# Kernel tuning notes

Measured on AMD Instinct MI355X. Metric: run time of the kernel, lower is better.

Reference implementation:

```python
import jax, jax.numpy as jnp
import numpy as np
from jax.scipy.special import logsumexp

NG, NF, NR, NW = 5, 5, 5, 4
STEP = 1 + NG + NF + NR            # 16 signatures per writer
M_OTH = NG + NF + NR               # comparisons per writer
MARGIN, RANDOM_MARGIN = 1.0, 1.5
ALPHA, BETA, P_W, R_W = 0.1, 1.0, 0.01, 0.01
GAMMA = 5.0                        # SoftDTW(gamma=5, bandwidth=int(0.1)=0 -> full DTW)
KNUM, KMUL = 5, 2.0
MAXLEN, FEAT = 512, 64
BIG = 1e10                         # finite stand-in for +inf (exp(-BIG/GAMMA) == 0 in f32)


def _pairwise_sqdist(X, Y):
    # X,Y: (B, L, F) -> (B, L, L) squared euclidean cost (SoftDTW distance func)
    xy = jnp.einsum('bif,bjf->bij', X, Y)
    d = (X * X).sum(-1)[:, :, None] + (Y * Y).sum(-1)[:, None, :] - 2.0 * xy
    return jnp.maximum(d, 0.0)


def _soft_dtw(D, la, lb):
    # Batched soft-DTW via anti-diagonal scan. Padded DP is causal, so
    # R[la, lb] only depends on D[:la, :lb]; padding never contaminates it.
    B, L, _ = D.shape
    ii = jnp.arange(1, L + 1)
    r2 = jnp.full((B, L + 1), BIG, D.dtype).at[:, 0].set(0.0)  # diag d=0: R[0,0]=0
    r1 = jnp.full((B, L + 1), BIG, D.dtype)                    # diag d=1: borders

    def step(carry, d):
        rp2, rp1 = carry
        j = d - ii
        valid = (j >= 1) & (j <= L)
        jc = jnp.clip(j, 1, L)
        Dd = D[:, ii - 1, jc - 1]                               # (B, L)
        # softmin(R[i-1,j], R[i,j-1], R[i-1,j-1]) = -g*logsumexp(-r/g)
        stack = jnp.stack([-rp1[:, :-1], -rp1[:, 1:], -rp2[:, :-1]]) / GAMMA
        smin = -GAMMA * logsumexp(stack, axis=0)
        vals = jnp.where(valid[None, :], Dd + smin, BIG)
        r_new = jnp.concatenate([jnp.full((B, 1), BIG, D.dtype), vals], axis=1)
        return (rp1, r_new), r_new

    _, R = jax.lax.scan(step, (r2, r1), jnp.arange(2, 2 * L + 1))
    # R: (2L-1, B, L+1); diag d stored at d-2, R[la, lb] sits at index la
    return R[la + lb - 2, jnp.arange(B), la]


def _mmd(src, tgt):
    # DAN-style multi-kernel gaussian MMD; signatures flattened to vectors
    b = src.shape[0]
    total = jnp.concatenate([src, tgt], axis=0)
    n = total.shape[0]
    sq = (total * total).sum(-1)
    l2 = jnp.maximum(sq[:, None] + sq[None, :] - 2.0 * (total @ total.T), 0.0)
    bw = jax.lax.stop_gradient(l2.sum()) / (n * n - n)
    bw = bw / KMUL ** (KNUM // 2)
    bws = bw * KMUL ** jnp.arange(KNUM, dtype=total.dtype)
    k = jnp.exp(-l2[None] / bws[:, None, None]).sum(0)
    return jnp.mean(k[:b, :b] + k[b:, b:] - k[:b, b:] - k[b:, :b])


def _forward(data, lens):
    w = jnp.arange(NW)
    anchor_idx = jnp.repeat(w * STEP, M_OTH)
    other_idx = (w[:, None] * STEP + 1 + jnp.arange(M_OTH)[None, :]).reshape(-1)
    D = _pairwise_sqdist(data[anchor_idx], data[other_idx])
    la, lb = lens[anchor_idx], lens[other_idx]
    r = _soft_dtw(D, la, lb)
    dists = (r / (la + lb).astype(data.dtype)).reshape(NW, M_OTH)  # avg pooling
    dist_g = dists[:, :NG]
    dist_n = dists[:, NG:]
    lk_s = jax.nn.relu(dist_g[:, :, None] + MARGIN - dist_n[:, None, :NF])
    lk_r = jax.nn.relu(dist_g[:, :, None] + RANDOM_MARGIN - dist_n[:, None, NF:])
    ca = dist_g.mean(1)
    cb = dist_n[:, :NW].mean(1)            # quirk of original: first nw negatives
    intra = (dist_g - ca[:, None]).sum(1)  # identically 0, kept for fidelity
    inter = jax.nn.relu(BETA - jnp.abs(ca - cb))
    nz_s = (lk_s > 0).sum((1, 2))
    nz_r = (lk_r > 0).sum((1, 2))
    lv = (lk_s.sum((1, 2)) + lk_r.sum((1, 2))) / (nz_s + nz_r + 1)
    # BCE over softmin pairs (dist_g[0], dist_r[j]) vs targets (1, 0):
    # softmin gives sm0 = sigmoid(dr - dg0); BCE = -(log sm0 + log(1-sm1))/2 = -log sm0
    logits = dist_n[:, NF:] - dist_g[:, 0:1]
    bce = -jnp.mean(jax.nn.log_sigmoid(logits), axis=1)
    total_loss = jnp.mean(bce + lv + intra * P_W + inter * R_W)
    # pairwise MMD over writers (i in 0..nw-1, j in 1..nw-1, i != j), nr random excluded
    pairs = np.array([(i, j) for i in range(NW) for j in range(1, NW) if i != j])
    seg = data.reshape(NW, STEP, MAXLEN, FEAT)[:, :STEP - NR]
    seg = seg.reshape(NW, STEP - NR, MAXLEN * FEAT)
    mmd_vals = jax.vmap(_mmd)(seg[pairs[:, 0]], seg[pairs[:, 1]])
    siz = NW * (NW + 1) // 2
    mmds = jnp.zeros((siz,), data.dtype).at[:pairs.shape[0]].set(mmd_vals)
    mmd1 = jnp.max(mmds) * ALPHA
    return total_loss + mmd1, nz_r.sum()


def setup_inputs():
    key = jax.random.key(0)
    k1, k2, k3 = jax.random.split(key, 3)
    data = jax.random.normal(k1, (NW * STEP, MAXLEN, FEAT), dtype=jnp.float32)
    lens = jax.random.randint(k2, (NW * STEP,), MAXLEN // 2, MAXLEN + 1, dtype=jnp.int32)
    target = jax.random.randint(k3, (NW * STEP,), 0, NW, dtype=jnp.int32)
    return {"data": data, "lens": lens, "target": target, "n_classes": 100}


def reference(data, lens, target, n_classes):
    # target / n_classes are unused in the original forward (sms is dead code)
    return _forward(data, lens)
```

## Files before the change

### kernel.cpp

```cpp
#include <hip/hip_runtime.h>
#include <math.h>

#define NG 5
#define NF 5
#define NR 5
#define NW 4
#define STEP 16
#define M_OTH 15
#define NB 60
#define L 512
#define FEAT 64
#define GAMMA 5.0f
#define SEGN 11
#define NSEG 44
#define SEGD 32768

#define C1   0.28853900817779268f
#define GLN2 3.4657359027997265f
#define BIGS 2.8853900e9f
#define BNDW 800
#define GRAM_BLK0 60

__global__ __launch_bounds__(256, 2) void sqdist_kernel(const float* __restrict__ data,
                                                        const int* __restrict__ lens,
                                                        float* __restrict__ DS) {
    int b = blockIdx.z;
    int w = b / M_OTH, m = b % M_OTH;
    int la = lens[w * STEP];
    int lb = lens[w * STEP + 1 + m];
    int ti = blockIdx.y * 128;
    int tj = blockIdx.x * 128;
    if (ti >= la || tj >= lb) return;

    const float* X = data + (size_t)(w * STEP) * L * FEAT;
    const float* Y = data + (size_t)(w * STEP + 1 + m) * L * FEAT;

    __shared__ float Xs[128][68];
    __shared__ float Ys[128][68];
    __shared__ float nx[128], ny[128];

    int t = threadIdx.y * 16 + threadIdx.x;
    #pragma unroll
    for (int k = 0; k < 8; ++k) {
        int idx = t + k * 256;
        int r = idx >> 4, c = (idx & 15) * 4;
        *(float4*)&Xs[r][c] = *(const float4*)(X + (size_t)(ti + r) * FEAT + c);
        *(float4*)&Ys[r][c] = *(const float4*)(Y + (size_t)(tj + r) * FEAT + c);
    }
    __syncthreads();
    {
        int r = t & 127;
        const float* row = (t < 128) ? Xs[r] : Ys[r];
        float s = 0.f;
        #pragma unroll
        for (int f = 0; f < 64; f += 4) {
            float4 v = *(const float4*)&row[f];
            s += v.x * v.x + v.y * v.y + v.z * v.z + v.w * v.w;
        }
        if (t < 128) nx[r] = s; else ny[r] = s;
    }
    __syncthreads();

    int tx = threadIdx.x, ty = threadIdx.y;
    float acc[8][8] = {};
    for (int f = 0; f < 64; f += 4) {
        float4 xv[8], yv[8];
        #pragma unroll
        for (int a = 0; a < 8; ++a) xv[a] = *(const float4*)&Xs[16 * a + tx][f];
        #pragma unroll
        for (int c = 0; c < 8; ++c) yv[c] = *(const float4*)&Ys[16 * c + ty][f];
        #pragma unroll
        for (int a = 0; a < 8; ++a)
            #pragma unroll
            for (int c = 0; c < 8; ++c)
                acc[a][c] += xv[a].x * yv[c].x + xv[a].y * yv[c].y +
                             xv[a].z * yv[c].z + xv[a].w * yv[c].w;
    }
    #pragma unroll
    for (int a = 0; a < 8; ++a) {
        int ii = ti + 16 * a + tx;
        float xn = nx[16 * a + tx];
        #pragma unroll
        for (int c = 0; c < 8; ++c) {
            int jj = tj + 16 * c + ty;
            float d = xn + ny[16 * c + ty] - 2.0f * acc[a][c];
            size_t idx = ((size_t)b * 512 + ((jj + (ii >> 1)) & 511)) * 512 + ii;
            DS[idx] = fmaxf(d, 0.0f) * C1;
        }
    }
}

__device__ __forceinline__ float dpp_shift_up1(float x) {
    int xi = __float_as_int(x);
    int sh  = __builtin_amdgcn_update_dpp(xi, xi, 0x111, 0xF, 0xF, false);
    int b15 = __builtin_amdgcn_update_dpp(xi, xi, 0x142, 0xF, 0xF, false);
    int lane = (int)(threadIdx.x & 63);
    int r = ((lane & 15) == 0) ? b15 : sh;
    return __int_as_float(r);
}

__device__ void gram_body(const float* __restrict__ data, float* __restrict__ Gm, int f) {
    int bx = 0, rem = f;
    for (int q = 0; q < 11; ++q) { int c = 11 - q; if (rem < c) { bx = q; break; } rem -= c; }
    int by = bx + rem;
    int t = threadIdx.x;
    int lane = t & 63, wv = t >> 6;
    const float* pa[4];
    const float* pb[4];
    #pragma unroll
    for (int i = 0; i < 4; ++i) {
        int sa = bx * 4 + i;
        int sb = by * 4 + i;
        pa[i] = data + (size_t)((sa / SEGN) * STEP + (sa % SEGN)) * SEGD;
        pb[i] = data + (size_t)((sb / SEGN) * STEP + (sb % SEGN)) * SEGD;
    }
    float acc[16] = {};
    for (int d = t * 4; d < SEGD; d += 1024) {
        float4 ra[4], rb[4];
        #pragma unroll
        for (int i = 0; i < 4; ++i) ra[i] = *(const float4*)(pa[i] + d);
        #pragma unroll
        for (int i = 0; i < 4; ++i) rb[i] = *(const float4*)(pb[i] + d);
        #pragma unroll
        for (int i = 0; i < 4; ++i)
            #pragma unroll
            for (int jj = 0; jj < 4; ++jj)
                acc[i * 4 + jj] += ra[i].x * rb[jj].x + ra[i].y * rb[jj].y +
                                   ra[i].z * rb[jj].z + ra[i].w * rb[jj].w;
    }
    #pragma unroll
    for (int i = 0; i < 16; ++i)
        #pragma unroll
        for (int s = 32; s > 0; s >>= 1)
            acc[i] += __shfl_xor(acc[i], s);
    __shared__ float part[4][16];
    if (lane == 0)
        #pragma unroll
        for (int i = 0; i < 16; ++i) part[wv][i] = acc[i];
    __syncthreads();
    if (t < 16) {
        float s = part[0][t] + part[1][t] + part[2][t] + part[3][t];
        int a = bx * 4 + (t >> 2), c = by * 4 + (t & 3);
        Gm[a * NSEG + c] = s;
        Gm[c * NSEG + a] = s;
    }
}

__global__ __launch_bounds__(256) void dtw_gram_kernel(const float* __restrict__ DS,
                                                       const int* __restrict__ lens,
                                                       const float* __restrict__ data,
                                                       float* __restrict__ res,
                                                       float* __restrict__ Gm) {
    int blk = blockIdx.x;
    if (blk >= GRAM_BLK0) { gram_body(data, Gm, blk - GRAM_BLK0); return; }

    int b = blk;
    int w_ = b / M_OTH, m = b % M_OTH;
    int la = lens[w_ * STEP];
    int lb = lens[w_ * STEP + 1 + m];
    int tid = threadIdx.x;
    int W = tid >> 6, l = tid & 63, G = tid;
    const float* Db = DS + (size_t)b * 512 * 512;

    __shared__ float bnd[3][BNDW];
    for (int k = tid; k < 3 * BNDW; k += 256)
        ((float*)bnd)[k] = __int_as_float(0x7FC00000);
    __syncthreads();

    int gstar = (la - 1) >> 1;
    int rstar = (la - 1) & 1;
    int tcap = lb + gstar - 1;
    if (64 * W > gstar) return;
    int gmax = min(64 * W + 63, gstar);
    int t0 = 64 * W;
    int tend = lb + gmax - 1;
    int needmax = lb + 64 * W - 1;
    bool pub = (W < 3);

    float nv0 = BIGS, nv1 = BIGS;
    float A0 = BIGS;
    float C0 = (G == 0) ? 0.0f : BIGS;
    float out = 0.0f;

    float2 ring[16];
    #pragma unroll
    for (int k = 0; k < 16; ++k)
        ring[k] = *(const float2*)&Db[(size_t)((t0 + k) & 511) * 512 + 2 * G];
    float ch[16];
    #pragma unroll
    for (int k = 0; k < 16; ++k) ch[k] = __int_as_float(0x7FC00000);

    int j = 1 - l;
    const float* bsrc = (W > 0) ? bnd[W - 1] : bnd[0];

    for (int t = t0; t <= tend; t += 16) {
        if (W > 0 && t <= needmax) {
            int lastIdx = min(t + 15, needmax);
            for (;;) {
                float chk = 0.f;
                #pragma unroll
                for (int k = 0; k < 16; ++k)
                    if (t + k <= needmax) chk += ch[k];
                if (!__builtin_isnan(chk)) break;
                float v = __hip_atomic_load(&bsrc[lastIdx], __ATOMIC_RELAXED,
                                            __HIP_MEMORY_SCOPE_WORKGROUP);
                while (__builtin_isnan(v)) {
                    __builtin_amdgcn_s_sleep(2);
                    v = __hip_atomic_load(&bsrc[lastIdx], __ATOMIC_RELAXED,
                                          __HIP_MEMORY_SCOPE_WORKGROUP);
                }
                __builtin_amdgcn_fence(__ATOMIC_ACQUIRE, "workgroup");
                #pragma unroll
                for (int k = 0; k < 4; ++k) {
                    float4 c = *(const float4*)&bsrc[t + 4 * k];
                    ch[4 * k] = c.x; ch[4 * k + 1] = c.y;
                    ch[4 * k + 2] = c.z; ch[4 * k + 3] = c.w;
                }
            }
        }
        #pragma unroll
        for (int k = 0; k < 16; ++k) {
            int tt = t + k;
            float l0 = BIGS;
            if (W > 0) l0 = (tt <= needmax) ? ch[k] : BIGS;
            A0 = (l == 0) ? l0 : A0;
            float D0 = ring[k].x, D1 = ring[k].y;
            ring[k] = *(const float2*)&Db[(size_t)((tt + 16) & 511) * 512 + 2 * G];
            float m2a = fminf(nv0, C0), mxa = fmaxf(nv0, C0);
            float E2a = 1.0f + __builtin_amdgcn_exp2f(m2a - mxa);
            float m2b = fminf(nv1, nv0), mxb = fmaxf(nv1, nv0);
            float E2b = 1.0f + __builtin_amdgcn_exp2f(m2b - mxb);
            float mn0 = fminf(A0, m2a);
            float s0 = __builtin_amdgcn_exp2f(mn0 - A0) +
                       E2a * __builtin_amdgcn_exp2f(mn0 - m2a);
            float t0v = D0 + (mn0 - __builtin_amdgcn_logf(s0));
            float mn1 = fminf(t0v, m2b);
            float s1 = __builtin_amdgcn_exp2f(mn1 - t0v) +
                       E2b * __builtin_amdgcn_exp2f(mn1 - m2b);
            float t1v = D1 + (mn1 - __builtin_amdgcn_logf(s1));
            bool valid = (unsigned)(j - 1) < (unsigned)L;
            nv0 = valid ? t0v : nv0;
            nv1 = valid ? t1v : nv1;
            if (tt == tcap) { if (G == gstar) out = rstar ? nv1 : nv0; }
            float up = dpp_shift_up1(nv1);
            if (pub && l == 63)
                __hip_atomic_store(&bnd[W][tt + 1], nv1, __ATOMIC_RELAXED,
                                   __HIP_MEMORY_SCOPE_WORKGROUP);
            C0 = A0;
            A0 = up;
            j += 1;
        }
        if (W > 0) {
            #pragma unroll
            for (int k = 0; k < 4; ++k) {
                float4 c = *(const float4*)&bsrc[t + 16 + 4 * k];
                ch[4 * k] = c.x; ch[4 * k + 1] = c.y;
                ch[4 * k + 2] = c.z; ch[4 * k + 3] = c.w;
            }
        }
    }
    if (G == gstar) res[b] = out * GLN2 / (float)(la + lb);
}

__global__ __launch_bounds__(512) void finalize_kernel(const float* __restrict__ res,
                                                       const float* __restrict__ G,
                                                       float* __restrict__ out) {
    __shared__ float wpart[9][8];
    __shared__ float bws[9];
    __shared__ float mmds[9];
    __shared__ float wloss[NW];
    __shared__ int   wnzr[NW];
    int t = threadIdx.x, lane = t & 63, wv = t >> 6;

    if (t < NW) {
        int w = t;
        float dg[NG], dn[NF + NR];
        for (int g = 0; g < NG; ++g) dg[g] = res[w * M_OTH + g];
        for (int q2 = 0; q2 < NF + NR; ++q2) dn[q2] = res[w * M_OTH + NG + q2];
        float sum_s = 0.f, sum_r = 0.f;
        int nzs = 0, nzr = 0;
        for (int g = 0; g < NG; ++g) {
            for (int f = 0; f < NF; ++f) {
                float v = dg[g] + 1.0f - dn[f];
                if (v > 0.f) { sum_s += v; nzs++; }
            }
            for (int r = 0; r < NR; ++r) {
                float v = dg[g] + 1.5f - dn[NF + r];
                if (v > 0.f) { sum_r += v; nzr++; }
            }
        }
        float ca = (dg[0] + dg[1] + dg[2] + dg[3] + dg[4]) / 5.0f;
        float cb = (dn[0] + dn[1] + dn[2] + dn[3]) * 0.25f;
        float intra = 0.f;
        for (int g = 0; g < NG; ++g) intra += dg[g] - ca;
        float inter = fmaxf(0.f, 1.0f - fabsf(ca - cb));
        float lv = (sum_s + sum_r) / (float)(nzs + nzr + 1);
        float bce = 0.f;
        for (int r = 0; r < NR; ++r) {
            float x = dn[NF + r] - dg[0];
            float ls = (x >= 0.f) ? -log1pf(expf(-x)) : (x - log1pf(expf(x)));
            bce += ls;
        }
        bce = -bce / 5.0f;
        wloss[w] = bce + lv + intra * 0.01f + inter * 0.01f;
        wnzr[w] = nzr;
    }

    const int pi[9] = {0, 0, 0, 1, 1, 2, 2, 3, 3};
    const int pj[9] = {1, 2, 3, 2, 3, 1, 3, 1, 2};
    int pp = t / 22, qq = t % 22;
    bool act = t < 484;
    float l2v[9];
    #pragma unroll
    for (int p = 0; p < 9; ++p) {
        float v = 0.f;
        if (act) {
            int wi = pi[p], wj = pj[p];
            int gp = (pp < 11) ? wi * SEGN + pp : wj * SEGN + (pp - 11);
            int gq = (qq < 11) ? wi * SEGN + qq : wj * SEGN + (qq - 11);
            v = fmaxf(G[gp * NSEG + gp] + G[gq * NSEG + gq] - 2.f * G[gp * NSEG + gq], 0.f);
        }
        l2v[p] = v;
    }
    #pragma unroll
    for (int p = 0; p < 9; ++p) {
        float r = l2v[p];
        #pragma unroll
        for (int s = 32; s > 0; s >>= 1) r += __shfl_xor(r, s);
        if (lane == 0) wpart[p][wv] = r;
    }
    __syncthreads();
    if (t < 9) {
        float s = 0.f;
        #pragma unroll
        for (int k = 0; k < 8; ++k) s += wpart[t][k];
        bws[t] = s * (1.0f / 462.0f) * 0.25f;
    }
    __syncthreads();
    float sgn = ((pp < 11) == (qq < 11)) ? 1.f : -1.f;
    #pragma unroll
    for (int p = 0; p < 9; ++p) {
        float kv = 0.f;
        if (act) {
            float x = -l2v[p] / bws[p];
            kv = sgn * (__expf(x) + __expf(x * 0.5f) + __expf(x * 0.25f) +
                        __expf(x * 0.125f) + __expf(x * 0.0625f));
        }
        #pragma unroll
        for (int s = 32; s > 0; s >>= 1) kv += __shfl_xor(kv, s);
        if (lane == 0) wpart[p][wv] = kv;
    }
    __syncthreads();
    if (t < 9) {
        float s = 0.f;
        #pragma unroll
        for (int k = 0; k < 8; ++k) s += wpart[t][k];
        mmds[t] = s / 121.0f;
    }
    __syncthreads();
    if (t == 0) {
        float loss = 0.25f * (wloss[0] + wloss[1] + wloss[2] + wloss[3]);
        float mx = 0.f;
        for (int p = 0; p < 9; ++p) mx = fmaxf(mx, mmds[p]);
        out[0] = loss + 0.1f * mx;
        out[1] = (float)(wnzr[0] + wnzr[1] + wnzr[2] + wnzr[3]);
    }
}

extern "C" void kernel_launch(void* const* d_in, const int* in_sizes, int n_in,
                              void* d_out, int out_size, void* d_ws, size_t ws_size,
                              hipStream_t stream) {
    const float* data = (const float*)d_in[0];
    const int* lens = (const int*)d_in[1];

    float* DS  = (float*)d_ws;
    float* res = DS + (size_t)NB * 512 * 512;
    float* G   = res + 64;
    float* out = (float*)d_out;

    dim3 g1(4, 4, NB), b1(16, 16);
    sqdist_kernel<<<g1, b1, 0, stream>>>(data, lens, DS);
    dtw_gram_kernel<<<GRAM_BLK0 + 66, 256, 0, stream>>>(DS, lens, data, res, G);
    finalize_kernel<<<1, 512, 0, stream>>>(res, G, out);
}
```

Before: 168.2 us.

## Move MMD Gram blocks into sqdist kernel and stage DS stores through LDS

The MMD Gram-matrix blocks move out of the DTW kernel and into the pairwise-distance kernel, so the latency-bound DTW launch has only DTW blocks. The skewed diagonal-layout writes of the cost matrix are first staged in shared memory and then written as contiguous float2 rows, replacing strided scalar global stores. This adds extra barriers and reuses the tile buffers for staging. Gram blocks now compete with the sqdist tiles for GPU resources.

```diff
diff --git a/kernel.cpp b/kernel.cpp
--- a/kernel.cpp
+++ b/kernel.cpp
@@ -19,27 +19,81 @@
 #define GLN2 3.4657359027997265f
 #define BIGS 2.8853900e9f
 #define BNDW 800
-#define GRAM_BLK0 60
-
-__global__ __launch_bounds__(256, 2) void sqdist_kernel(const float* __restrict__ data,
-                                                        const int* __restrict__ lens,
-                                                        float* __restrict__ DS) {
-    int b = blockIdx.z;
+#define GRAM_BLKS 66
+
+__device__ void gram_body(const float* __restrict__ data, float* __restrict__ Gm, int f) {
+    int bx = 0, rem = f;
+    for (int q = 0; q < 11; ++q) { int c = 11 - q; if (rem < c) { bx = q; break; } rem -= c; }
+    int by = bx + rem;
+    int t = threadIdx.y * 16 + threadIdx.x;
+    int lane = t & 63, wv = t >> 6;
+    const float* pa[4];
+    const float* pb[4];
+    #pragma unroll
+    for (int i = 0; i < 4; ++i) {
+        int sa = bx * 4 + i;
+        int sb = by * 4 + i;
+        pa[i] = data + (size_t)((sa / SEGN) * STEP + (sa % SEGN)) * SEGD;
+        pb[i] = data + (size_t)((sb / SEGN) * STEP + (sb % SEGN)) * SEGD;
+    }
+    float acc[16] = {};
+    for (int d = t * 4; d < SEGD; d += 1024) {
+        float4 ra[4], rb[4];
+        #pragma unroll
+        for (int i = 0; i < 4; ++i) ra[i] = *(const float4*)(pa[i] + d);
+        #pragma unroll
+        for (int i = 0; i < 4; ++i) rb[i] = *(const float4*)(pb[i] + d);
+        #pragma unroll
+        for (int i = 0; i < 4; ++i)
+            #pragma unroll
+            for (int jj = 0; jj < 4; ++jj)
+                acc[i * 4 + jj] += ra[i].x * rb[jj].x + ra[i].y * rb[jj].y +
+                                   ra[i].z * rb[jj].z + ra[i].w * rb[jj].w;
+    }
+    #pragma unroll
+    for (int i = 0; i < 16; ++i)
+        #pragma unroll
+        for (int s = 32; s > 0; s >>= 1)
+            acc[i] += __shfl_xor(acc[i], s);
+    __shared__ float part[4][16];
+    if (lane == 0)
+        #pragma unroll
+        for (int i = 0; i < 16; ++i) part[wv][i] = acc[i];
+    __syncthreads();
+    if (t < 16) {
+        float s = part[0][t] + part[1][t] + part[2][t] + part[3][t];
+        int a = bx * 4 + (t >> 2), c = by * 4 + (t & 3);
+        Gm[a * NSEG + c] = s;
+        Gm[c * NSEG + a] = s;
+    }
+}
+
+__global__ __launch_bounds__(256, 2) void pre_kernel(const float* __restrict__ data,
+                                                     const int* __restrict__ lens,
+                                                     float* __restrict__ DS,
+                                                     float* __restrict__ Gm) {
+    __shared__ float pool[2 * 128 * 68];
+    __shared__ float nx[128], ny[128];
+
+    int blk = blockIdx.x;
+    if (blk < GRAM_BLKS) { gram_body(data, Gm, blk); return; }
+
+    int s_ = blk - GRAM_BLKS;
+    int b  = s_ >> 4;
+    int rr = (s_ & 15) >> 2, cc = s_ & 3;
+    int ti = rr * 128, tj = cc * 128;
     int w = b / M_OTH, m = b % M_OTH;
     int la = lens[w * STEP];
     int lb = lens[w * STEP + 1 + m];
-    int ti = blockIdx.y * 128;
-    int tj = blockIdx.x * 128;
     if (ti >= la || tj >= lb) return;
 
     const float* X = data + (size_t)(w * STEP) * L * FEAT;
     const float* Y = data + (size_t)(w * STEP + 1 + m) * L * FEAT;
-
-    __shared__ float Xs[128][68];
-    __shared__ float Ys[128][68];
-    __shared__ float nx[128], ny[128];
-
-    int t = threadIdx.y * 16 + threadIdx.x;
+    float (*Xs)[68] = (float(*)[68])pool;
+    float (*Ys)[68] = (float(*)[68])(pool + 128 * 68);
+
+    int tx = threadIdx.x, ty = threadIdx.y;
+    int t = ty * 16 + tx;
     #pragma unroll
     for (int k = 0; k < 8; ++k) {
         int idx = t + k * 256;
@@ -61,7 +115,6 @@
     }
     __syncthreads();
 
-    int tx = threadIdx.x, ty = threadIdx.y;
     float acc[8][8] = {};
     for (int f = 0; f < 64; f += 4) {
         float4 xv[8], yv[8];
@@ -76,16 +129,38 @@
                 acc[a][c] += xv[a].x * yv[c].x + xv[a].y * yv[c].y +
                              xv[a].z * yv[c].z + xv[a].w * yv[c].w;
     }
-    #pragma unroll
-    for (int a = 0; a < 8; ++a) {
-        int ii = ti + 16 * a + tx;
-        float xn = nx[16 * a + tx];
-        #pragma unroll
-        for (int c = 0; c < 8; ++c) {
-            int jj = tj + 16 * c + ty;
-            float d = xn + ny[16 * c + ty] - 2.0f * acc[a][c];
-            size_t idx = ((size_t)b * 512 + ((jj + (ii >> 1)) & 511)) * 512 + ii;
-            DS[idx] = fmaxf(d, 0.0f) * C1;
+
+    float (*St)[132] = (float(*)[132])pool;
+    int rowT = t >> 1, halfT = t & 1;
+    size_t dbase = (size_t)b * 512 * 512;
+    #pragma unroll
+    for (int h = 0; h < 2; ++h) {
+        __syncthreads();
+        #pragma unroll
+        for (int a = 0; a < 8; ++a) {
+            float xn = nx[16 * a + tx];
+            int iiL = 16 * a + tx;
+            #pragma unroll
+            for (int c4 = 0; c4 < 4; ++c4) {
+                int c = 4 * h + c4;
+                int jjL = 16 * c + ty;
+                float d = xn + ny[16 * c + ty] - 2.0f * acc[a][c];
+                int r = (jjL - 64 * h) + (iiL >> 1);
+                St[r][iiL] = fmaxf(d, 0.0f) * C1;
+            }
+        }
+        __syncthreads();
+        {
+            int r = rowT;
+            int lo = max(0, r - 63), hi = min(63, r);
+            int np = hi - lo + 1;
+            int nh = (np + 1) >> 1;
+            int p0 = lo + halfT * nh;
+            int p1 = (halfT ? hi + 1 : lo + nh);
+            int grow = (tj + 64 * h + (ti >> 1) + r) & 511;
+            float* dst = DS + dbase + (size_t)grow * 512 + ti;
+            for (int p = p0; p < p1; ++p)
+                *(float2*)(dst + 2 * p) = *(const float2*)&St[r][2 * p];
         }
     }
 }
@@ -99,62 +174,10 @@
     return __int_as_float(r);
 }
 
-__device__ void gram_body(const float* __restrict__ data, float* __restrict__ Gm, int f) {
-    int bx = 0, rem = f;
-    for (int q = 0; q < 11; ++q) { int c = 11 - q; if (rem < c) { bx = q; break; } rem -= c; }
-    int by = bx + rem;
-    int t = threadIdx.x;
-    int lane = t & 63, wv = t >> 6;
-    const float* pa[4];
-    const float* pb[4];
-    #pragma unroll
-    for (int i = 0; i < 4; ++i) {
-        int sa = bx * 4 + i;
-        int sb = by * 4 + i;
-        pa[i] = data + (size_t)((sa / SEGN) * STEP + (sa % SEGN)) * SEGD;
-        pb[i] = data + (size_t)((sb / SEGN) * STEP + (sb % SEGN)) * SEGD;
-    }
-    float acc[16] = {};
-    for (int d = t * 4; d < SEGD; d += 1024) {
-        float4 ra[4], rb[4];
-        #pragma unroll
-        for (int i = 0; i < 4; ++i) ra[i] = *(const float4*)(pa[i] + d);
-        #pragma unroll
-        for (int i = 0; i < 4; ++i) rb[i] = *(const float4*)(pb[i] + d);
-        #pragma unroll
-        for (int i = 0; i < 4; ++i)
-            #pragma unroll
-            for (int jj = 0; jj < 4; ++jj)
-                acc[i * 4 + jj] += ra[i].x * rb[jj].x + ra[i].y * rb[jj].y +
-                                   ra[i].z * rb[jj].z + ra[i].w * rb[jj].w;
-    }
-    #pragma unroll
-    for (int i = 0; i < 16; ++i)
-        #pragma unroll
-        for (int s = 32; s > 0; s >>= 1)
-            acc[i] += __shfl_xor(acc[i], s);
-    __shared__ float part[4][16];
-    if (lane == 0)
-        #pragma unroll
-        for (int i = 0; i < 16; ++i) part[wv][i] = acc[i];
-    __syncthreads();
-    if (t < 16) {
-        float s = part[0][t] + part[1][t] + part[2][t] + part[3][t];
-        int a = bx * 4 + (t >> 2), c = by * 4 + (t & 3);
-        Gm[a * NSEG + c] = s;
-        Gm[c * NSEG + a] = s;
-    }
-}
-
-__global__ __launch_bounds__(256) void dtw_gram_kernel(const float* __restrict__ DS,
-                                                       const int* __restrict__ lens,
-                                                       const float* __restrict__ data,
-                                                       float* __restrict__ res,
-                                                       float* __restrict__ Gm) {
-    int blk = blockIdx.x;
-    if (blk >= GRAM_BLK0) { gram_body(data, Gm, blk - GRAM_BLK0); return; }
-
-    int b = blk;
+__global__ __launch_bounds__(256) void dtw_kernel(const float* __restrict__ DS,
+                                                  const int* __restrict__ lens,
+                                                  float* __restrict__ res) {
+    int b = blockIdx.x;
     int w_ = b / M_OTH, m = b % M_OTH;
     int la = lens[w_ * STEP];
     int lb = lens[w_ * STEP + 1 + m];
@@ -378,8 +401,8 @@
     float* G   = res + 64;
     float* out = (float*)d_out;
 
-    dim3 g1(4, 4, NB), b1(16, 16);
-    sqdist_kernel<<<g1, b1, 0, stream>>>(data, lens, DS);
-    dtw_gram_kernel<<<GRAM_BLK0 + 66, 256, 0, stream>>>(DS, lens, data, res, G);
+    dim3 b1(16, 16);
+    pre_kernel<<<GRAM_BLKS + NB * 16, b1, 0, stream>>>(data, lens, DS, G);
+    dtw_kernel<<<NB, 256, 0, stream>>>(DS, lens, res);
     finalize_kernel<<<1, 512, 0, stream>>>(res, G, out);
 }
```

New measurement: 182.2 us. +8.4%, slower.
